# Performance work log

Hardware: AMD Instinct MI355X
Metric: run time of the kernel (lower is better)

Reference implementation:

```python
import jax, jax.numpy as jnp
import numpy as np

EPS = 1e-5

def conv3d(x, w):
    # x: [B,C,D,H,W], w: [O,I,3,3,3], stride 1, padding 1 (size preserving)
    return jax.lax.conv_general_dilated(
        x, w, window_strides=(1, 1, 1),
        padding=((1, 1), (1, 1), (1, 1)),
        dimension_numbers=('NCDHW', 'OIDHW', 'NCDHW'))

def deconv3d(x, w):
    # ConvTranspose3d(k=3, s=1, p=1) == conv3d with spatially flipped kernel, in/out swapped
    # torch ConvTranspose3d weight layout: [in, out, kD, kH, kW]
    wc = jnp.flip(w, axis=(2, 3, 4)).transpose(1, 0, 2, 3, 4)
    return conv3d(x, wc)

def batchnorm(x, bn):
    # bn: [4, C] rows = (gamma, beta, running_mean, running_var); inference mode
    g, b, m, v = bn[0], bn[1], bn[2], bn[3]
    scale = g * jax.lax.rsqrt(v + EPS)
    shift = b - m * scale
    return x * scale[None, :, None, None, None] + shift[None, :, None, None, None]

def qrnn_scan(Z, F, reverse):
    # gated linear recurrence h_t = f_t*h_{t-1} + (1-f_t)*z_t over depth axis (dim 2)
    Zs = jnp.moveaxis(Z, 2, 0)  # [D,B,C,H,W]
    Fs = jnp.moveaxis(F, 2, 0)
    def step(h, zf):
        z, f = zf
        h = f * h + (1.0 - f) * z
        return h, h
    h0 = jnp.zeros_like(Zs[0])  # h=None in torch == h=0 since f*0 vanishes
    _, hs = jax.lax.scan(step, h0, (Zs, Fs), reverse=reverse)
    return jnp.moveaxis(hs, 0, 2)

def qrnn_layer(x, w, bn, hidden, reverse, upsample, transpose):
    if upsample:
        # nn.Upsample(scale_factor=(1,2,2)) nearest
        x = jnp.repeat(jnp.repeat(x, 2, axis=3), 2, axis=4)
    g = deconv3d(x, w) if transpose else conv3d(x, w)
    g = batchnorm(g, bn)
    Z, F = g[:, :hidden], g[:, hidden:]
    return qrnn_scan(jnp.tanh(Z), jax.nn.sigmoid(F), reverse)

def setup_inputs():
    key = jax.random.key(0)
    ks = jax.random.split(key, 12)
    B, D = 4, 31
    x = jax.random.normal(ks[0], (B, 64, D, 32, 32), jnp.float32)
    xs2 = jax.random.normal(ks[1], (B, 32, D, 64, 64), jnp.float32)
    xs1 = jax.random.normal(ks[2], (B, 32, D, 64, 64), jnp.float32)
    xs0 = jax.random.normal(ks[3], (B, 16, D, 128, 128), jnp.float32)
    def wconv(k, shape):
        fan_in = shape[1] * 27
        return jax.random.normal(k, shape, jnp.float32) / np.float32(np.sqrt(fan_in))
    # layer0: UpsampleConv3d 64 -> 32 hidden (gates 64): Conv3d weight [64,64,3,3,3]
    w0 = wconv(ks[4], (64, 64, 3, 3, 3))
    # layer1: DeConv3D 32 -> 32 hidden (gates 64): ConvTranspose weight [in=32,out=64,3,3,3]
    w1 = wconv(ks[5], (32, 64, 3, 3, 3))
    # layer2: UpsampleConv3d 32 -> 16 hidden (gates 32): Conv3d weight [32,32,3,3,3]
    w2 = wconv(ks[6], (32, 32, 3, 3, 3))
    # layer3: DeConv3D 16 -> 16 hidden (gates 32): ConvTranspose weight [16,32,3,3,3]
    w3 = wconv(ks[7], (16, 32, 3, 3, 3))
    def mkbn(k, c):
        k1, k2, k3, k4 = jax.random.split(k, 4)
        return jnp.stack([
            jax.random.uniform(k1, (c,), jnp.float32, 0.5, 1.5),   # gamma
            jax.random.normal(k2, (c,), jnp.float32) * 0.1,        # beta
            jax.random.normal(k3, (c,), jnp.float32) * 0.1,        # running mean
            jax.random.uniform(k4, (c,), jnp.float32, 0.5, 1.5)])  # running var
    bn0 = mkbn(ks[8], 64)
    bn1 = mkbn(ks[9], 64)
    bn2 = mkbn(ks[10], 32)
    bn3 = mkbn(ks[11], 32)
    return dict(x=x, xs0=xs0, xs1=xs1, xs2=xs2,
                w0=w0, w1=w1, w2=w2, w3=w3,
                bn0=bn0, bn1=bn1, bn2=bn2, bn3=bn3)

def reference(x, xs0, xs1, xs2, w0, w1, w2, w3, bn0, bn1, bn2, bn3):
    # QRNN3DDecoder.forward with has_ad=True, reverse=False; scan direction alternates.
    # xs are popped last-first: xs2, xs1, xs0.
    h = qrnn_layer(x, w0, bn0, 32, False, True, False)          # upsample conv -> [B,32,D,64,64]
    h = qrnn_layer(h + xs2, w1, bn1, 32, True, False, True)     # deconv        -> [B,32,D,64,64]
    h = qrnn_layer(h + xs1, w2, bn2, 16, False, True, False)    # upsample conv -> [B,16,D,128,128]
    h = qrnn_layer(h + xs0, w3, bn3, 16, True, False, True)     # deconv        -> [B,16,D,128,128]
    return h
```

## Files before the change

### kernel.cpp

```cpp
#include <hip/hip_runtime.h>
#include <math.h>

#define BB 4
#define DD 31

typedef _Float16 half8 __attribute__((ext_vector_type(8)));
typedef float f32x4 __attribute__((ext_vector_type(4)));

__device__ __forceinline__ int swz(int b) { return b ^ (((b >> 7) & 7) << 4); }
__device__ __forceinline__ half8 ldswz(const _Float16* lin, int byteoff) {
    return *(const half8*)((const char*)lin + swz(byteoff));
}
__device__ __forceinline__ void stswz(_Float16* lin, int byteoff, half8 v) {
    *(half8*)((char*)lin + swz(byteoff)) = v;
}
__device__ __forceinline__ float fast_tanh(float y) {
    float e = __expf(2.f * y);
    return 1.f - 2.f * __builtin_amdgcn_rcpf(e + 1.f);
}
__device__ __forceinline__ float fast_sigmoid(float y) {
    return __builtin_amdgcn_rcpf(1.f + __expf(-y));
}


__global__ void bnprep(const float* __restrict__ bn, int C, float* __restrict__ sh) {
    int c = threadIdx.x;
    if (c >= C) return;
    float g = bn[c], b = bn[C + c], m = bn[2 * C + c], v = bn[3 * C + c];
    sh[c] = b - m * (g * rsqrtf(v + 1e-5f));
}

__global__ void wprep(const float* __restrict__ src, const float* __restrict__ bn,
                      _Float16* __restrict__ dst, int CIN, int COUT, int KS, int CS, int tr) {
    int idx = blockIdx.x * 256 + threadIdx.x;
    int total = CS * KS * 1024;
    if (idx >= total) return;
    int ki = idx & 31;
    int c16 = (idx >> 5) & 15;
    int n = (idx >> 9) & 1;
    int ko = (idx >> 10) % KS;
    int q = idx / (KS * 1024);
    int co = n * (COUT / 2) + q * 16 + c16;
    int k = ko * 32 + ki;
    float v = 0.f;
    if (k < 27 * CIN) {
        int tap = k / CIN, ci = k % CIN;
        v = tr ? src[((size_t)ci * COUT + co) * 27 + (26 - tap)]
               : src[((size_t)co * CIN + ci) * 27 + tap];
        v *= bn[co] * rsqrtf(bn[3 * COUT + co] + 1e-5f);
    }
    dst[idx] = (_Float16)v;
}

__global__ void wprep_up(const float* __restrict__ src, const float* __restrict__ bn,
                         _Float16* __restrict__ dst, int CIN, int COUT, int KS, int CS) {
    int idx = blockIdx.x * 256 + threadIdx.x;
    int total = CS * 4 * KS * 1024;
    if (idx >= total) return;
    int ki = idx & 31;
    int c16 = (idx >> 5) & 15;
    int n = (idx >> 9) & 1;
    int ko = (idx >> 10) % KS;
    int par = (idx / (KS * 1024)) & 3;
    int q = idx / (KS * 4096);
    int co = n * (COUT / 2) + q * 16 + c16;
    int k = ko * 32 + ki;
    int ci = k % CIN, tap = k / CIN;
    int kd = tap >> 2, ih = (tap >> 1) & 1, iw = tap & 1;
    int ph = par >> 1, pw = par & 1;
    const float c[2][2][3] = {{{1, 0, 0}, {0, 1, 1}}, {{1, 1, 0}, {0, 0, 1}}};
    float v = 0.f;
    for (int kh = 0; kh < 3; ++kh)
        for (int kw = 0; kw < 3; ++kw)
            v += c[ph][ih][kh] * c[pw][iw][kw] *
                 src[((size_t)co * CIN + ci) * 27 + kd * 9 + kh * 3 + kw];
    v *= bn[co] * rsqrtf(bn[3 * COUT + co] + 1e-5f);
    dst[idx] = (_Float16)v;
}

__global__ __launch_bounds__(256) void xconv(const float* __restrict__ src,
                                             _Float16* __restrict__ dst) {
    int idx = blockIdx.x * 256 + threadIdx.x;
    if (idx >= 4 * 31 * 1024 * 8) return;
    int cb = idx & 7;
    int pos = (idx >> 3) & 1023;
    int bd = idx >> 13;
    int d = bd % 31, b = bd / 31;
    half8 v;
#pragma unroll
    for (int j = 0; j < 8; ++j)
        v[j] = (_Float16)src[(((size_t)b * 64 + cb * 8 + j) * 31 + d) * 1024 + pos];
    *(half8*)(dst + ((size_t)bd * 1024 + pos) * 64 + cb * 8) = v;
}

template <int CIN, int S, int HID, int KS, int NF, int CS, int REV, int LAST>
__global__ __launch_bounds__(256, 2) void fconv(
    const _Float16* __restrict__ inp,
    const _Float16* __restrict__ wq,
    const float* __restrict__ bnsh,
    const float* __restrict__ xs,
    _Float16* __restrict__ hout,
    float* __restrict__ fout) {

    constexpr int IW = 18;
    constexpr int TH = 4 * NF;
    constexpr int IHP = TH + 2;
    constexpr int NC8 = CIN / 8;
    constexpr int P8 = IHP * IW * NC8;
    constexpr int NST = (P8 + 255) / 256;
    constexpr int PLANEB = IHP * IW * CIN * 2;

    __shared__ __align__(16) _Float16 lin[4 * IHP * IW * CIN];

    const int tid = threadIdx.x;
    const int lane = tid & 63;
    const int wv = tid >> 6;
    const int col = lane & 15;
    const int grp = lane >> 4;

    const int w0 = blockIdx.x * 16;
    const int h0 = blockIdx.y * TH;
    const int b = blockIdx.z / CS;
    const int q = blockIdx.z % CS;
    const size_t bbase = (size_t)b * DD;

    const float shz = bnsh[q * 16 + col];
    const float shf = bnsh[HID + q * 16 + col];
    const int hc = q * 16 + col;
    const _Float16* wqb = wq + (size_t)q * KS * 1024;

    auto stage_now = [&](int dz) {
        int slot = (dz + 8) & 3;
        for (int idx = tid; idx < P8; idx += 256) {
            int c8 = idx % NC8;
            int pos = idx / NC8;
            int ih = pos / IW, iw = pos % IW;
            int gh = h0 - 1 + ih, gw = w0 - 1 + iw;
            half8 v = {0, 0, 0, 0, 0, 0, 0, 0};
            if ((unsigned)dz < (unsigned)DD && (unsigned)gh < (unsigned)S &&
                (unsigned)gw < (unsigned)S)
                v = *(const half8*)(inp + (((bbase + dz) * S + gh) * S + gw) * CIN + c8 * 8);
            stswz(lin, slot * PLANEB + (pos * CIN + c8 * 8) * 2, v);
        }
    };

    constexpr int dir = REV ? -1 : 1;
    const int d0 = REV ? DD - 1 : 0;
    stage_now(d0 - dir);
    stage_now(d0);
    stage_now(d0 + dir);
    __syncthreads();

    float hst[NF][4];
#pragma unroll
    for (int f = 0; f < NF; ++f)
#pragma unroll
        for (int r = 0; r < 4; ++r) hst[f][r] = 0.f;

    for (int t = 0; t < DD; ++t) {
        const int d = d0 + dir * t;
        const int dzl = d + 2 * dir;

        half8 sv[NST];
#pragma unroll
        for (int i = 0; i < NST; ++i) {
            int idx = tid + i * 256;
            half8 v = {0, 0, 0, 0, 0, 0, 0, 0};
            if (idx < P8) {
                int c8 = idx % NC8;
                int pos = idx / NC8;
                int ih = pos / IW, iw = pos % IW;
                int gh = h0 - 1 + ih, gw = w0 - 1 + iw;
                if ((unsigned)dzl < (unsigned)DD && (unsigned)gh < (unsigned)S &&
                    (unsigned)gw < (unsigned)S)
                    v = *(const half8*)(inp +
                        (((bbase + dzl) * S + gh) * S + gw) * CIN + c8 * 8);
            }
            sv[i] = v;
        }

        f32x4 acc[NF][2];
#pragma unroll
        for (int f = 0; f < NF; ++f) {
            acc[f][0] = {0.f, 0.f, 0.f, 0.f};
            acc[f][1] = {0.f, 0.f, 0.f, 0.f};
        }
#pragma unroll
        for (int ko = 0; ko < KS; ++ko) {
            int kd, kh, kw, ci;
            if (CIN >= 32) {
                int tap = (ko * 32) / CIN;
                kd = tap / 9; kh = (tap / 3) % 3; kw = tap % 3;
                ci = (ko * 32) % CIN + grp * 8;
            } else {
                int t0 = (2 * ko < 27) ? 2 * ko : 26;
                int t1 = (2 * ko + 1 < 27) ? 2 * ko + 1 : 26;
                int hi = grp >> 1;
                kd = hi ? t1 / 9 : t0 / 9;
                kh = hi ? (t1 / 3) % 3 : (t0 / 3) % 3;
                kw = hi ? t1 % 3 : t0 % 3;
                ci = (grp & 1) * 8;
            }
            int slot = (d + kd + 7) & 3;
            int iw = col + kw;
            half8 a[NF];
#pragma unroll
            for (int f = 0; f < NF; ++f)
                a[f] = ldswz(lin, slot * PLANEB +
                             (((wv * NF + f + kh) * IW + iw) * CIN + ci) * 2);
            half8 bf0 = *(const half8*)(wqb + ko * 1024 + col * 32 + grp * 8);
            half8 bf1 = *(const half8*)(wqb + ko * 1024 + 512 + col * 32 + grp * 8);
#pragma unroll
            for (int f = 0; f < NF; ++f) {
                acc[f][0] = __builtin_amdgcn_mfma_f32_16x16x32_f16(a[f], bf0, acc[f][0], 0, 0, 0);
                acc[f][1] = __builtin_amdgcn_mfma_f32_16x16x32_f16(a[f], bf1, acc[f][1], 0, 0, 0);
            }
        }

        {
            int slot = (dzl + 8) & 3;
#pragma unroll
            for (int i = 0; i < NST; ++i) {
                int idx = tid + i * 256;
                if (idx < P8) {
                    int c8 = idx % NC8;
                    int pos = idx / NC8;
                    stswz(lin, slot * PLANEB + (pos * CIN + c8 * 8) * 2, sv[i]);
                }
            }
        }

#pragma unroll
        for (int f = 0; f < NF; ++f) {
            int h = h0 + wv * NF + f;
#pragma unroll
            for (int r = 0; r < 4; ++r) {
                int w = w0 + grp * 4 + r;
                size_t sp = (size_t)h * S + w;
                float z = fast_tanh(acc[f][0][r] + shz);
                float fg = fast_sigmoid(acc[f][1][r] + shf);
                hst[f][r] = fg * hst[f][r] + (1.f - fg) * z;
                if (LAST) {
                    fout[(((size_t)b * HID + hc) * DD + d) * ((size_t)S * S) + sp] = hst[f][r];
                } else {
                    float xv = xs[(((size_t)b * HID + hc) * DD + d) * ((size_t)S * S) + sp];
                    hout[((bbase + d) * ((size_t)S * S) + sp) * HID + hc] =
                        (_Float16)(hst[f][r] + xv);
                }
            }
        }
        __syncthreads();
    }
}

template <int CIN, int S, int HID, int KS, int NF, int CS, int REV, int LAST>
__global__ __launch_bounds__(256, 2) void fconv_up(
    const _Float16* __restrict__ inp,
    const _Float16* __restrict__ wq,
    const float* __restrict__ bnsh,
    const float* __restrict__ xs,
    _Float16* __restrict__ hout,
    float* __restrict__ fout) {

    constexpr int SIN = S / 2;
    constexpr int IW = 18;
    constexpr int IHP = NF + 2;
    constexpr int NC8 = CIN / 8;
    constexpr int P8 = IHP * IW * NC8;
    constexpr int NST = (P8 + 255) / 256;
    constexpr int PLANEB = IHP * IW * CIN * 2;

    __shared__ __align__(16) _Float16 lin[4 * IHP * IW * CIN];

    const int tid = threadIdx.x;
    const int lane = tid & 63;
    const int wv = tid >> 6;
    const int col = lane & 15;
    const int grp = lane >> 4;
    const int ph = wv >> 1, pw = wv & 1;

    const int bwp = blockIdx.x * 16;
    const int bhp = blockIdx.y * NF;
    const int b = blockIdx.z / CS;
    const int q = blockIdx.z % CS;
    const size_t bbase = (size_t)b * DD;

    const float shz = bnsh[q * 16 + col];
    const float shf = bnsh[HID + q * 16 + col];
    const int hc = q * 16 + col;
    const _Float16* wqb = wq + ((size_t)(q * 4 + wv) * KS) * 1024;

    auto stage_now = [&](int dz) {
        int slot = (dz + 8) & 3;
        for (int idx = tid; idx < P8; idx += 256) {
            int c8 = idx % NC8;
            int pos = idx / NC8;
            int ih = pos / IW, iw = pos % IW;
            int gh = bhp - 1 + ih, gw = bwp - 1 + iw;
            half8 v = {0, 0, 0, 0, 0, 0, 0, 0};
            if ((unsigned)dz < (unsigned)DD && (unsigned)gh < (unsigned)SIN &&
                (unsigned)gw < (unsigned)SIN)
                v = *(const half8*)(inp + (((bbase + dz) * SIN + gh) * SIN + gw) * CIN + c8 * 8);
            stswz(lin, slot * PLANEB + (pos * CIN + c8 * 8) * 2, v);
        }
    };

    constexpr int dir = REV ? -1 : 1;
    const int d0 = REV ? DD - 1 : 0;
    stage_now(d0 - dir);
    stage_now(d0);
    stage_now(d0 + dir);
    __syncthreads();

    float hst[NF][4];
#pragma unroll
    for (int f = 0; f < NF; ++f)
#pragma unroll
        for (int r = 0; r < 4; ++r) hst[f][r] = 0.f;

    for (int t = 0; t < DD; ++t) {
        const int d = d0 + dir * t;
        const int dzl = d + 2 * dir;

        half8 sv[NST];
#pragma unroll
        for (int i = 0; i < NST; ++i) {
            int idx = tid + i * 256;
            half8 v = {0, 0, 0, 0, 0, 0, 0, 0};
            if (idx < P8) {
                int c8 = idx % NC8;
                int pos = idx / NC8;
                int ih = pos / IW, iw = pos % IW;
                int gh = bhp - 1 + ih, gw = bwp - 1 + iw;
                if ((unsigned)dzl < (unsigned)DD && (unsigned)gh < (unsigned)SIN &&
                    (unsigned)gw < (unsigned)SIN)
                    v = *(const half8*)(inp +
                        (((bbase + dzl) * SIN + gh) * SIN + gw) * CIN + c8 * 8);
            }
            sv[i] = v;
        }

        f32x4 acc[NF][2];
#pragma unroll
        for (int f = 0; f < NF; ++f) {
            acc[f][0] = {0.f, 0.f, 0.f, 0.f};
            acc[f][1] = {0.f, 0.f, 0.f, 0.f};
        }
#pragma unroll
        for (int ko = 0; ko < KS; ++ko) {
            int tap = (ko * 32) / CIN;
            int ci = (ko * 32) % CIN + grp * 8;
            int kd = tap >> 2, ihh = (tap >> 1) & 1, iwk = tap & 1;
            int slot = (d + kd + 7) & 3;
            int lcol = col + iwk + pw;
            int row0 = ihh + ph;
            half8 a[NF];
#pragma unroll
            for (int f = 0; f < NF; ++f)
                a[f] = ldswz(lin, slot * PLANEB +
                             ((((row0 + f) * IW) + lcol) * CIN + ci) * 2);
            half8 bf0 = *(const half8*)(wqb + ko * 1024 + col * 32 + grp * 8);
            half8 bf1 = *(const half8*)(wqb + ko * 1024 + 512 + col * 32 + grp * 8);
#pragma unroll
            for (int f = 0; f < NF; ++f) {
                acc[f][0] = __builtin_amdgcn_mfma_f32_16x16x32_f16(a[f], bf0, acc[f][0], 0, 0, 0);
                acc[f][1] = __builtin_amdgcn_mfma_f32_16x16x32_f16(a[f], bf1, acc[f][1], 0, 0, 0);
            }
        }

        {
            int slot = (dzl + 8) & 3;
#pragma unroll
            for (int i = 0; i < NST; ++i) {
                int idx = tid + i * 256;
                if (idx < P8) {
                    int c8 = idx % NC8;
                    int pos = idx / NC8;
                    stswz(lin, slot * PLANEB + (pos * CIN + c8 * 8) * 2, sv[i]);
                }
            }
        }

#pragma unroll
        for (int f = 0; f < NF; ++f) {
            int h = 2 * (bhp + f) + ph;
#pragma unroll
            for (int r = 0; r < 4; ++r) {
                int w = 2 * (bwp + grp * 4 + r) + pw;
                size_t sp = (size_t)h * S + w;
                float z = fast_tanh(acc[f][0][r] + shz);
                float fg = fast_sigmoid(acc[f][1][r] + shf);
                hst[f][r] = fg * hst[f][r] + (1.f - fg) * z;
                if (LAST) {
                    fout[(((size_t)b * HID + hc) * DD + d) * ((size_t)S * S) + sp] = hst[f][r];
                } else {
                    float xv = xs[(((size_t)b * HID + hc) * DD + d) * ((size_t)S * S) + sp];
                    hout[((bbase + d) * ((size_t)S * S) + sp) * HID + hc] =
                        (_Float16)(hst[f][r] + xv);
                }
            }
        }
        __syncthreads();
    }
}

extern "C" void kernel_launch(void* const* d_in, const int* in_sizes, int n_in,
                              void* d_out, int out_size, void* d_ws, size_t ws_size,
                              hipStream_t stream) {
    const float* x   = (const float*)d_in[0];
    const float* xs0 = (const float*)d_in[1];
    const float* xs1 = (const float*)d_in[2];
    const float* xs2 = (const float*)d_in[3];
    const float* w0  = (const float*)d_in[4];
    const float* w1  = (const float*)d_in[5];
    const float* w2  = (const float*)d_in[6];
    const float* w3  = (const float*)d_in[7];
    const float* bn0 = (const float*)d_in[8];
    const float* bn1 = (const float*)d_in[9];
    const float* bn2 = (const float*)d_in[10];
    const float* bn3 = (const float*)d_in[11];
    float* out = (float*)d_out;

    char* p = (char*)d_ws;
    _Float16* xf   = (_Float16*)p; p += (size_t)124 * 1024 * 64 * 2;
    _Float16* hA   = (_Float16*)p; p += (size_t)124 * 4096 * 32 * 2;
    _Float16* hA2  = (_Float16*)p; p += (size_t)124 * 4096 * 32 * 2;
    _Float16* hB   = (_Float16*)p; p += (size_t)124 * 16384 * 16 * 2;
    _Float16* wq0u = (_Float16*)p; p += (size_t)2 * 4 * 24 * 1024 * 2;
    _Float16* wq1  = (_Float16*)p; p += (size_t)2 * 27 * 1024 * 2;
    _Float16* wq2u = (_Float16*)p; p += (size_t)4 * 12 * 1024 * 2;
    _Float16* wq3  = (_Float16*)p; p += (size_t)14 * 1024 * 2;
    float* sh0 = (float*)p; p += 64 * 4;
    float* sh1 = (float*)p; p += 64 * 4;
    float* sh2 = (float*)p; p += 64 * 4;
    float* sh3 = (float*)p; p += 64 * 4;

    xconv<<<(4 * 31 * 1024 * 8 + 255) / 256, 256, 0, stream>>>(x, xf);
    wprep_up<<<(2 * 4 * 24 * 1024 + 255) / 256, 256, 0, stream>>>(w0, bn0, wq0u, 64, 64, 24, 2);
    wprep<<<(2 * 27 * 1024 + 255) / 256, 256, 0, stream>>>(w1, bn1, wq1, 32, 64, 27, 2, 1);
    wprep_up<<<(4 * 12 * 1024 + 255) / 256, 256, 0, stream>>>(w2, bn2, wq2u, 32, 32, 12, 1);
    wprep<<<(14 * 1024 + 255) / 256, 256, 0, stream>>>(w3, bn3, wq3, 16, 32, 14, 1, 1);
    bnprep<<<1, 64, 0, stream>>>(bn0, 64, sh0);
    bnprep<<<1, 64, 0, stream>>>(bn1, 64, sh1);
    bnprep<<<1, 64, 0, stream>>>(bn2, 32, sh2);
    bnprep<<<1, 64, 0, stream>>>(bn3, 32, sh3);

    fconv_up<64, 64, 32, 24, 1, 2, 0, 0><<<dim3(2, 32, BB * 2), 256, 0, stream>>>(
        xf, wq0u, sh0, xs2, hA, nullptr);
    fconv<32, 64, 32, 27, 1, 2, 1, 0><<<dim3(4, 16, BB * 2), 256, 0, stream>>>(
        hA, wq1, sh1, xs1, hA2, nullptr);
    fconv_up<32, 128, 16, 12, 2, 1, 0, 0><<<dim3(4, 32, BB), 256, 0, stream>>>(
        hA2, wq2u, sh2, xs0, hB, nullptr);
    fconv<16, 128, 16, 14, 2, 1, 1, 1><<<dim3(8, 16, BB), 256, 0, stream>>>(
        hB, wq3, sh3, nullptr, nullptr, out);
}
```

Baseline: 602.8 us.

## Split layer0 into parallel conv plus scan, stage weights in LDS, re-grid layers

Layer 0 is split into a depth-parallel conv_up kernel, which writes activated gates to a new fp16 buffer, and a separate qscan kernel. The aim is more parallelism than the serial fused depth loop gives. The fused conv kernels now keep three slab slots instead of four and copy the weights (full or half) into LDS once per block, instead of reading them from global memory inside the MFMA loop. Layer 2 is re-gridded so each block handles one parity and a 4-row tile. The cost is an extra gate-tensor round trip through global memory, an extra __syncthreads per depth step, and larger LDS use that may lower occupancy.

```diff
diff --git a/kernel.cpp b/kernel.cpp
--- a/kernel.cpp
+++ b/kernel.cpp
@@ -52,18 +52,41 @@
     dst[idx] = (_Float16)v;
 }
 
-__global__ void wprep_up(const float* __restrict__ src, const float* __restrict__ bn,
-                         _Float16* __restrict__ dst, int CIN, int COUT, int KS, int CS) {
+__global__ void wprep_upA(const float* __restrict__ src, const float* __restrict__ bn,
+                          _Float16* __restrict__ dst, int CIN, int COUT) {
+    const int KS = 12 * CIN / 32;
     int idx = blockIdx.x * 256 + threadIdx.x;
-    int total = CS * 4 * KS * 1024;
+    int total = 4 * KS * 32 * COUT;
+    if (idx >= total) return;
+    int ki = idx % 32;
+    int co = (idx / 32) % COUT;
+    int ko = (idx / (32 * COUT)) % KS;
+    int par = idx / (32 * COUT * KS);
+    int k = ko * 32 + ki;
+    int ci = k % CIN, tap = k / CIN;
+    int kd = tap >> 2, ih = (tap >> 1) & 1, iw = tap & 1;
+    int ph = par >> 1, pw = par & 1;
+    const float c[2][2][3] = {{{1, 0, 0}, {0, 1, 1}}, {{1, 1, 0}, {0, 0, 1}}};
+    float v = 0.f;
+    for (int kh = 0; kh < 3; ++kh)
+        for (int kw = 0; kw < 3; ++kw)
+            v += c[ph][ih][kh] * c[pw][iw][kw] *
+                 src[((size_t)co * CIN + ci) * 27 + kd * 9 + kh * 3 + kw];
+    v *= bn[co] * rsqrtf(bn[3 * COUT + co] + 1e-5f);
+    dst[(((size_t)par * KS + ko) * COUT + co) * 32 + ki] = (_Float16)v;
+}
+
+__global__ void wprep_upB(const float* __restrict__ src, const float* __restrict__ bn,
+                          _Float16* __restrict__ dst, int CIN, int COUT, int KS) {
+    int idx = blockIdx.x * 256 + threadIdx.x;
+    int total = 4 * KS * 1024;
     if (idx >= total) return;
     int ki = idx & 31;
     int c16 = (idx >> 5) & 15;
     int n = (idx >> 9) & 1;
     int ko = (idx >> 10) % KS;
-    int par = (idx / (KS * 1024)) & 3;
-    int q = idx / (KS * 4096);
-    int co = n * (COUT / 2) + q * 16 + c16;
+    int par = idx / (KS * 1024);
+    int co = n * (COUT / 2) + c16;
     int k = ko * 32 + ki;
     int ci = k % CIN, tap = k / CIN;
     int kd = tap >> 2, ih = (tap >> 1) & 1, iw = tap & 1;
@@ -93,8 +116,145 @@
     *(half8*)(dst + ((size_t)bd * 1024 + pos) * 64 + cb * 8) = v;
 }
 
-template <int CIN, int S, int HID, int KS, int NF, int CS, int REV, int LAST>
-__global__ __launch_bounds__(256, 2) void fconv(
+template <int CIN, int COUT, int S, int MINW>
+__global__ __launch_bounds__(256, MINW) void conv_up(
+    const _Float16* __restrict__ inp,
+    const _Float16* __restrict__ wqu,
+    const float* __restrict__ bnsh,
+    _Float16* __restrict__ gout) {
+
+    constexpr int SIN = S / 2;
+    constexpr int KS = 12 * CIN / 32;
+    constexpr int NCB = COUT / 16;
+    constexpr int NC8 = CIN / 8;
+    constexpr int IH = 6, IW = 18;
+    constexpr int PATCH = 3 * IH * IW;
+
+    __shared__ __align__(16) _Float16 lin[PATCH * CIN];
+
+    const int tid = threadIdx.x;
+    const int lane = tid & 63;
+    const int wv = tid >> 6;
+    const int col = lane & 15;
+    const int grp = lane >> 4;
+    const int ph = wv >> 1, pw = wv & 1;
+
+    const int bwp = blockIdx.x * 16;
+    const int bhp = blockIdx.y * 4;
+    const int bz = blockIdx.z;
+    const int d = bz % DD;
+
+    for (int idx = tid; idx < PATCH * NC8; idx += 256) {
+        int c8 = idx % NC8;
+        int pos = idx / NC8;
+        int iwp = pos % IW, t = pos / IW;
+        int ihp = t % IH, kd = t / IH;
+        int dz = d + kd - 1, gh = bhp - 1 + ihp, gw = bwp - 1 + iwp;
+        half8 v = {0, 0, 0, 0, 0, 0, 0, 0};
+        if ((unsigned)dz < (unsigned)DD && (unsigned)gh < (unsigned)SIN &&
+            (unsigned)gw < (unsigned)SIN)
+            v = *(const half8*)(inp +
+                (((size_t)(bz + kd - 1) * SIN + gh) * SIN + gw) * CIN + c8 * 8);
+        *(half8*)((char*)lin + swz((pos * CIN + c8 * 8) * 2)) = v;
+    }
+    __syncthreads();
+
+    f32x4 acc[4][NCB];
+#pragma unroll
+    for (int f = 0; f < 4; ++f)
+#pragma unroll
+        for (int n = 0; n < NCB; ++n) acc[f][n] = {0.f, 0.f, 0.f, 0.f};
+
+    const _Float16* wqp = wqu + (size_t)(ph * 2 + pw) * KS * COUT * 32;
+
+#pragma unroll
+    for (int ko = 0; ko < KS; ++ko) {
+        int tap = (ko * 32) / CIN;
+        int ci = (ko * 32) % CIN + grp * 8;
+        int kd = tap >> 2, ih = (tap >> 1) & 1, iwk = tap & 1;
+
+        int lcol = col + iwk + pw;
+        int r0 = ih + ph;
+        int cb = ((kd * IH + r0) * IW + lcol) * CIN + ci;
+        half8 a[4];
+#pragma unroll
+        for (int f = 0; f < 4; ++f)
+            a[f] = ldswz(lin, (cb + f * IW * CIN) * 2);
+
+        half8 bfr[NCB];
+#pragma unroll
+        for (int n = 0; n < NCB; ++n)
+            bfr[n] = *(const half8*)(wqp + ((ko * COUT + n * 16 + col) * 32 + grp * 8));
+#pragma unroll
+        for (int f = 0; f < 4; ++f)
+#pragma unroll
+            for (int n = 0; n < NCB; ++n)
+                acc[f][n] = __builtin_amdgcn_mfma_f32_16x16x32_f16(a[f], bfr[n],
+                                                                   acc[f][n], 0, 0, 0);
+    }
+
+    const size_t obase = (size_t)bz * S * S * COUT;
+#pragma unroll
+    for (int n = 0; n < NCB; ++n) {
+        int co = n * 16 + col;
+        float sh = bnsh[co];
+#pragma unroll
+        for (int f = 0; f < 4; ++f) {
+            int h = 2 * (bhp + f) + ph;
+#pragma unroll
+            for (int r = 0; r < 4; ++r) {
+                int w = 2 * (bwp + grp * 4 + r) + pw;
+                float y = acc[f][n][r] + sh;
+                float v = (n < NCB / 2) ? fast_tanh(y) : fast_sigmoid(y);
+                gout[obase + ((size_t)h * S + w) * COUT + co] = (_Float16)v;
+            }
+        }
+    }
+}
+
+template <int H, int HW, int LAST>
+__global__ __launch_bounds__(256) void qscan(
+    const _Float16* __restrict__ g, const float* __restrict__ xs,
+    _Float16* __restrict__ hout, float* __restrict__ fout, int rev) {
+    constexpr int NCB = H / 8;
+    int idx = blockIdx.x * 256 + threadIdx.x;
+    if (idx >= BB * HW * NCB) return;
+    int cb = idx % NCB;
+    int hw = (idx / NCB) % HW;
+    int b = idx / (NCB * HW);
+    int c0 = cb * 8;
+
+    float h[8];
+#pragma unroll
+    for (int j = 0; j < 8; ++j) h[j] = 0.f;
+
+    for (int t = 0; t < DD; ++t) {
+        int d = rev ? (DD - 1 - t) : t;
+        const _Float16* gp = g + ((size_t)(b * DD + d) * HW + hw) * (2 * H);
+        half8 z8 = *(const half8*)(gp + c0);
+        half8 f8 = *(const half8*)(gp + H + c0);
+        if (LAST) {
+#pragma unroll
+            for (int j = 0; j < 8; ++j) {
+                float fv = (float)f8[j];
+                h[j] = fv * h[j] + (1.f - fv) * (float)z8[j];
+                fout[(((size_t)b * H + c0 + j) * DD + d) * HW + hw] = h[j];
+            }
+        } else {
+            half8 o;
+#pragma unroll
+            for (int j = 0; j < 8; ++j) {
+                float fv = (float)f8[j];
+                h[j] = fv * h[j] + (1.f - fv) * (float)z8[j];
+                o[j] = (_Float16)(h[j] + xs[(((size_t)b * H + c0 + j) * DD + d) * HW + hw]);
+            }
+            *(half8*)(hout + ((size_t)(b * DD + d) * HW + hw) * H + c0) = o;
+        }
+    }
+}
+
+template <int CIN, int S, int HID, int KS, int NF, int CS, int REV, int LAST, int FULLW>
+__global__ __launch_bounds__(256, 2) void fconv3(
     const _Float16* __restrict__ inp,
     const _Float16* __restrict__ wq,
     const float* __restrict__ bnsh,
@@ -109,8 +269,10 @@
     constexpr int P8 = IHP * IW * NC8;
     constexpr int NST = (P8 + 255) / 256;
     constexpr int PLANEB = IHP * IW * CIN * 2;
-
-    __shared__ __align__(16) _Float16 lin[4 * IHP * IW * CIN];
+    constexpr int LWB = 3 * PLANEB;
+    constexpr int WH = KS * (FULLW ? 1024 : 512);
+
+    __shared__ __align__(16) _Float16 lds[(LWB / 2) + WH];
 
     const int tid = threadIdx.x;
     const int lane = tid & 63;
@@ -130,7 +292,7 @@
     const _Float16* wqb = wq + (size_t)q * KS * 1024;
 
     auto stage_now = [&](int dz) {
-        int slot = (dz + 8) & 3;
+        int slot = (dz + 33) % 3;
         for (int idx = tid; idx < P8; idx += 256) {
             int c8 = idx % NC8;
             int pos = idx / NC8;
@@ -140,7 +302,7 @@
             if ((unsigned)dz < (unsigned)DD && (unsigned)gh < (unsigned)S &&
                 (unsigned)gw < (unsigned)S)
                 v = *(const half8*)(inp + (((bbase + dz) * S + gh) * S + gw) * CIN + c8 * 8);
-            stswz(lin, slot * PLANEB + (pos * CIN + c8 * 8) * 2, v);
+            stswz(lds, slot * PLANEB + (pos * CIN + c8 * 8) * 2, v);
         }
     };
 
@@ -149,6 +311,11 @@
     stage_now(d0 - dir);
     stage_now(d0);
     stage_now(d0 + dir);
+    for (int i = tid; i < WH / 8; i += 256) {
+        int srcHalf = FULLW ? i * 8 : ((i >> 6) * 1024 + (i & 63) * 8);
+        half8 v = *(const half8*)(wqb + srcHalf);
+        stswz(lds, LWB + i * 16, v);
+    }
     __syncthreads();
 
     float hst[NF][4];
@@ -160,6 +327,10 @@
     for (int t = 0; t < DD; ++t) {
         const int d = d0 + dir * t;
         const int dzl = d + 2 * dir;
+        const int sm = (d - 1 + 33) % 3;
+        const int s0 = (d + 33) % 3;
+        const int sp = (d + 1 + 33) % 3;
+        const int scommit = REV ? sp : sm;
 
         half8 sv[NST];
 #pragma unroll
@@ -201,15 +372,19 @@
                 kw = hi ? t1 % 3 : t0 % 3;
                 ci = (grp & 1) * 8;
             }
-            int slot = (d + kd + 7) & 3;
+            int slot = kd == 0 ? sm : (kd == 1 ? s0 : sp);
             int iw = col + kw;
             half8 a[NF];
 #pragma unroll
             for (int f = 0; f < NF; ++f)
-                a[f] = ldswz(lin, slot * PLANEB +
+                a[f] = ldswz(lds, slot * PLANEB +
                              (((wv * NF + f + kh) * IW + iw) * CIN + ci) * 2);
-            half8 bf0 = *(const half8*)(wqb + ko * 1024 + col * 32 + grp * 8);
-            half8 bf1 = *(const half8*)(wqb + ko * 1024 + 512 + col * 32 + grp * 8);
+            half8 bf0 = ldswz(lds, LWB + (ko * (FULLW ? 1024 : 512) + col * 32 + grp * 8) * 2);
+            half8 bf1;
+            if (FULLW)
+                bf1 = ldswz(lds, LWB + (ko * 1024 + 512 + col * 32 + grp * 8) * 2);
+            else
+                bf1 = *(const half8*)(wqb + ko * 1024 + 512 + col * 32 + grp * 8);
 #pragma unroll
             for (int f = 0; f < NF; ++f) {
                 acc[f][0] = __builtin_amdgcn_mfma_f32_16x16x32_f16(a[f], bf0, acc[f][0], 0, 0, 0);
@@ -217,16 +392,14 @@
             }
         }
 
-        {
-            int slot = (dzl + 8) & 3;
-#pragma unroll
-            for (int i = 0; i < NST; ++i) {
-                int idx = tid + i * 256;
-                if (idx < P8) {
-                    int c8 = idx % NC8;
-                    int pos = idx / NC8;
-                    stswz(lin, slot * PLANEB + (pos * CIN + c8 * 8) * 2, sv[i]);
-                }
+        __syncthreads();
+#pragma unroll
+        for (int i = 0; i < NST; ++i) {
+            int idx = tid + i * 256;
+            if (idx < P8) {
+                int c8 = idx % NC8;
+                int pos = idx / NC8;
+                stswz(lds, scommit * PLANEB + (pos * CIN + c8 * 8) * 2, sv[i]);
             }
         }
 
@@ -236,15 +409,15 @@
 #pragma unroll
             for (int r = 0; r < 4; ++r) {
                 int w = w0 + grp * 4 + r;
-                size_t sp = (size_t)h * S + w;
+                size_t sp2 = (size_t)h * S + w;
                 float z = fast_tanh(acc[f][0][r] + shz);
                 float fg = fast_sigmoid(acc[f][1][r] + shf);
                 hst[f][r] = fg * hst[f][r] + (1.f - fg) * z;
                 if (LAST) {
-                    fout[(((size_t)b * HID + hc) * DD + d) * ((size_t)S * S) + sp] = hst[f][r];
+                    fout[(((size_t)b * HID + hc) * DD + d) * ((size_t)S * S) + sp2] = hst[f][r];
                 } else {
-                    float xv = xs[(((size_t)b * HID + hc) * DD + d) * ((size_t)S * S) + sp];
-                    hout[((bbase + d) * ((size_t)S * S) + sp) * HID + hc] =
+                    float xv = xs[(((size_t)b * HID + hc) * DD + d) * ((size_t)S * S) + sp2];
+                    hout[((bbase + d) * ((size_t)S * S) + sp2) * HID + hc] =
                         (_Float16)(hst[f][r] + xv);
                 }
             }
@@ -253,8 +426,8 @@
     }
 }
 
-template <int CIN, int S, int HID, int KS, int NF, int CS, int REV, int LAST>
-__global__ __launch_bounds__(256, 2) void fconv_up(
+template <int CIN, int S, int HID, int KS, int REV, int LAST>
+__global__ __launch_bounds__(256, 2) void fconv_up1(
     const _Float16* __restrict__ inp,
     const _Float16* __restrict__ wq,
     const float* __restrict__ bnsh,
@@ -264,34 +437,36 @@
 
     constexpr int SIN = S / 2;
     constexpr int IW = 18;
-    constexpr int IHP = NF + 2;
+    constexpr int IHP = 6;
     constexpr int NC8 = CIN / 8;
     constexpr int P8 = IHP * IW * NC8;
     constexpr int NST = (P8 + 255) / 256;
     constexpr int PLANEB = IHP * IW * CIN * 2;
-
-    __shared__ __align__(16) _Float16 lin[4 * IHP * IW * CIN];
+    constexpr int LWB = 3 * PLANEB;
+    constexpr int WH = KS * 1024;
+
+    __shared__ __align__(16) _Float16 lds[(LWB / 2) + WH];
 
     const int tid = threadIdx.x;
     const int lane = tid & 63;
     const int wv = tid >> 6;
     const int col = lane & 15;
     const int grp = lane >> 4;
-    const int ph = wv >> 1, pw = wv & 1;
 
     const int bwp = blockIdx.x * 16;
-    const int bhp = blockIdx.y * NF;
-    const int b = blockIdx.z / CS;
-    const int q = blockIdx.z % CS;
+    const int bhp = blockIdx.y * 4;
+    const int par = blockIdx.z & 3;
+    const int b = blockIdx.z >> 2;
+    const int ph = par >> 1, pw = par & 1;
     const size_t bbase = (size_t)b * DD;
 
-    const float shz = bnsh[q * 16 + col];
-    const float shf = bnsh[HID + q * 16 + col];
-    const int hc = q * 16 + col;
-    const _Float16* wqb = wq + ((size_t)(q * 4 + wv) * KS) * 1024;
+    const float shz = bnsh[col];
+    const float shf = bnsh[HID + col];
+    const int hc = col;
+    const _Float16* wqb = wq + (size_t)par * KS * 1024;
 
     auto stage_now = [&](int dz) {
-        int slot = (dz + 8) & 3;
+        int slot = (dz + 33) % 3;
         for (int idx = tid; idx < P8; idx += 256) {
             int c8 = idx % NC8;
             int pos = idx / NC8;
@@ -301,7 +476,7 @@
             if ((unsigned)dz < (unsigned)DD && (unsigned)gh < (unsigned)SIN &&
                 (unsigned)gw < (unsigned)SIN)
                 v = *(const half8*)(inp + (((bbase + dz) * SIN + gh) * SIN + gw) * CIN + c8 * 8);
-            stswz(lin, slot * PLANEB + (pos * CIN + c8 * 8) * 2, v);
+            stswz(lds, slot * PLANEB + (pos * CIN + c8 * 8) * 2, v);
         }
     };
 
@@ -310,17 +485,23 @@
     stage_now(d0 - dir);
     stage_now(d0);
     stage_now(d0 + dir);
+    for (int i = tid; i < WH / 8; i += 256) {
+        half8 v = *(const half8*)(wqb + i * 8);
+        stswz(lds, LWB + i * 16, v);
+    }
     __syncthreads();
 
-    float hst[NF][4];
-#pragma unroll
-    for (int f = 0; f < NF; ++f)
-#pragma unroll
-        for (int r = 0; r < 4; ++r) hst[f][r] = 0.f;
+    float hst[4];
+#pragma unroll
+    for (int r = 0; r < 4; ++r) hst[r] = 0.f;
 
     for (int t = 0; t < DD; ++t) {
         const int d = d0 + dir * t;
         const int dzl = d + 2 * dir;
+        const int sm = (d - 1 + 33) % 3;
+        const int s0 = (d + 33) % 3;
+        const int sp = (d + 1 + 33) % 3;
+        const int scommit = REV ? sp : sm;
 
         half8 sv[NST];
 #pragma unroll
@@ -340,64 +521,48 @@
             sv[i] = v;
         }
 
-        f32x4 acc[NF][2];
-#pragma unroll
-        for (int f = 0; f < NF; ++f) {
-            acc[f][0] = {0.f, 0.f, 0.f, 0.f};
-            acc[f][1] = {0.f, 0.f, 0.f, 0.f};
-        }
+        f32x4 accz = {0.f, 0.f, 0.f, 0.f};
+        f32x4 accf = {0.f, 0.f, 0.f, 0.f};
 #pragma unroll
         for (int ko = 0; ko < KS; ++ko) {
             int tap = (ko * 32) / CIN;
             int ci = (ko * 32) % CIN + grp * 8;
             int kd = tap >> 2, ihh = (tap >> 1) & 1, iwk = tap & 1;
-            int slot = (d + kd + 7) & 3;
+            int slot = kd == 0 ? sm : (kd == 1 ? s0 : sp);
             int lcol = col + iwk + pw;
-            int row0 = ihh + ph;
-            half8 a[NF];
-#pragma unroll
-            for (int f = 0; f < NF; ++f)
-                a[f] = ldswz(lin, slot * PLANEB +
-                             ((((row0 + f) * IW) + lcol) * CIN + ci) * 2);
-            half8 bf0 = *(const half8*)(wqb + ko * 1024 + col * 32 + grp * 8);
-            half8 bf1 = *(const half8*)(wqb + ko * 1024 + 512 + col * 32 + grp * 8);
-#pragma unroll
-            for (int f = 0; f < NF; ++f) {
-                acc[f][0] = __builtin_amdgcn_mfma_f32_16x16x32_f16(a[f], bf0, acc[f][0], 0, 0, 0);
-                acc[f][1] = __builtin_amdgcn_mfma_f32_16x16x32_f16(a[f], bf1, acc[f][1], 0, 0, 0);
-            }
-        }
-
-        {
-            int slot = (dzl + 8) & 3;
-#pragma unroll
-            for (int i = 0; i < NST; ++i) {
-                int idx = tid + i * 256;
-                if (idx < P8) {
-                    int c8 = idx % NC8;
-                    int pos = idx / NC8;
-                    stswz(lin, slot * PLANEB + (pos * CIN + c8 * 8) * 2, sv[i]);
-                }
-            }
-        }
-
-#pragma unroll
-        for (int f = 0; f < NF; ++f) {
-            int h = 2 * (bhp + f) + ph;
-#pragma unroll
-            for (int r = 0; r < 4; ++r) {
-                int w = 2 * (bwp + grp * 4 + r) + pw;
-                size_t sp = (size_t)h * S + w;
-                float z = fast_tanh(acc[f][0][r] + shz);
-                float fg = fast_sigmoid(acc[f][1][r] + shf);
-                hst[f][r] = fg * hst[f][r] + (1.f - fg) * z;
-                if (LAST) {
-                    fout[(((size_t)b * HID + hc) * DD + d) * ((size_t)S * S) + sp] = hst[f][r];
-                } else {
-                    float xv = xs[(((size_t)b * HID + hc) * DD + d) * ((size_t)S * S) + sp];
-                    hout[((bbase + d) * ((size_t)S * S) + sp) * HID + hc] =
-                        (_Float16)(hst[f][r] + xv);
-                }
+            int row = wv + ihh + ph;
+            half8 a = ldswz(lds, slot * PLANEB + ((row * IW + lcol) * CIN + ci) * 2);
+            half8 bf0 = ldswz(lds, LWB + (ko * 1024 + col * 32 + grp * 8) * 2);
+            half8 bf1 = ldswz(lds, LWB + (ko * 1024 + 512 + col * 32 + grp * 8) * 2);
+            accz = __builtin_amdgcn_mfma_f32_16x16x32_f16(a, bf0, accz, 0, 0, 0);
+            accf = __builtin_amdgcn_mfma_f32_16x16x32_f16(a, bf1, accf, 0, 0, 0);
+        }
+
+        __syncthreads();
+#pragma unroll
+        for (int i = 0; i < NST; ++i) {
+            int idx = tid + i * 256;
+            if (idx < P8) {
+                int c8 = idx % NC8;
+                int pos = idx / NC8;
+                stswz(lds, scommit * PLANEB + (pos * CIN + c8 * 8) * 2, sv[i]);
+            }
+        }
+
+        int h = 2 * (bhp + wv) + ph;
+#pragma unroll
+        for (int r = 0; r < 4; ++r) {
+            int w = 2 * (bwp + grp * 4 + r) + pw;
+            size_t sp2 = (size_t)h * S + w;
+            float z = fast_tanh(accz[r] + shz);
+            float fg = fast_sigmoid(accf[r] + shf);
+            hst[r] = fg * hst[r] + (1.f - fg) * z;
+            if (LAST) {
+                fout[(((size_t)b * HID + hc) * DD + d) * ((size_t)S * S) + sp2] = hst[r];
+            } else {
+                float xv = xs[(((size_t)b * HID + hc) * DD + d) * ((size_t)S * S) + sp2];
+                hout[((bbase + d) * ((size_t)S * S) + sp2) * HID + hc] =
+                    (_Float16)(hst[r] + xv);
             }
         }
         __syncthreads();
@@ -423,10 +588,11 @@
 
     char* p = (char*)d_ws;
     _Float16* xf   = (_Float16*)p; p += (size_t)124 * 1024 * 64 * 2;
+    _Float16* gA   = (_Float16*)p; p += (size_t)124 * 4096 * 64 * 2;
     _Float16* hA   = (_Float16*)p; p += (size_t)124 * 4096 * 32 * 2;
     _Float16* hA2  = (_Float16*)p; p += (size_t)124 * 4096 * 32 * 2;
     _Float16* hB   = (_Float16*)p; p += (size_t)124 * 16384 * 16 * 2;
-    _Float16* wq0u = (_Float16*)p; p += (size_t)2 * 4 * 24 * 1024 * 2;
+    _Float16* wq0u = (_Float16*)p; p += (size_t)4 * 24 * 64 * 32 * 2;
     _Float16* wq1  = (_Float16*)p; p += (size_t)2 * 27 * 1024 * 2;
     _Float16* wq2u = (_Float16*)p; p += (size_t)4 * 12 * 1024 * 2;
     _Float16* wq3  = (_Float16*)p; p += (size_t)14 * 1024 * 2;
@@ -436,21 +602,24 @@
     float* sh3 = (float*)p; p += 64 * 4;
 
     xconv<<<(4 * 31 * 1024 * 8 + 255) / 256, 256, 0, stream>>>(x, xf);
-    wprep_up<<<(2 * 4 * 24 * 1024 + 255) / 256, 256, 0, stream>>>(w0, bn0, wq0u, 64, 64, 24, 2);
+    wprep_upA<<<(4 * 24 * 32 * 64 + 255) / 256, 256, 0, stream>>>(w0, bn0, wq0u, 64, 64);
     wprep<<<(2 * 27 * 1024 + 255) / 256, 256, 0, stream>>>(w1, bn1, wq1, 32, 64, 27, 2, 1);
-    wprep_up<<<(4 * 12 * 1024 + 255) / 256, 256, 0, stream>>>(w2, bn2, wq2u, 32, 32, 12, 1);
+    wprep_upB<<<(4 * 12 * 1024 + 255) / 256, 256, 0, stream>>>(w2, bn2, wq2u, 32, 32, 12);
     wprep<<<(14 * 1024 + 255) / 256, 256, 0, stream>>>(w3, bn3, wq3, 16, 32, 14, 1, 1);
     bnprep<<<1, 64, 0, stream>>>(bn0, 64, sh0);
     bnprep<<<1, 64, 0, stream>>>(bn1, 64, sh1);
     bnprep<<<1, 64, 0, stream>>>(bn2, 32, sh2);
     bnprep<<<1, 64, 0, stream>>>(bn3, 32, sh3);
 
-    fconv_up<64, 64, 32, 24, 1, 2, 0, 0><<<dim3(2, 32, BB * 2), 256, 0, stream>>>(
-        xf, wq0u, sh0, xs2, hA, nullptr);
-    fconv<32, 64, 32, 27, 1, 2, 1, 0><<<dim3(4, 16, BB * 2), 256, 0, stream>>>(
+    conv_up<64, 64, 64, 3><<<dim3(2, 8, BB * DD), 256, 0, stream>>>(xf, wq0u, sh0, gA);
+    qscan<32, 4096, 0><<<(BB * 4096 * 4 + 255) / 256, 256, 0, stream>>>(gA, xs2, hA, nullptr, 0);
+
+    fconv3<32, 64, 32, 27, 1, 2, 1, 0, 0><<<dim3(4, 16, BB * 2), 256, 0, stream>>>(
         hA, wq1, sh1, xs1, hA2, nullptr);
-    fconv_up<32, 128, 16, 12, 2, 1, 0, 0><<<dim3(4, 32, BB), 256, 0, stream>>>(
+
+    fconv_up1<32, 128, 16, 12, 0, 0><<<dim3(4, 16, BB * 4), 256, 0, stream>>>(
         hA2, wq2u, sh2, xs0, hB, nullptr);
-    fconv<16, 128, 16, 14, 2, 1, 1, 1><<<dim3(8, 16, BB), 256, 0, stream>>>(
+
+    fconv3<16, 128, 16, 14, 2, 1, 1, 1, 1><<<dim3(8, 16, BB), 256, 0, stream>>>(
         hB, wq3, sh3, nullptr, nullptr, out);
 }
```

Result: slower. 906.3 us (+50.3%).
